# Kernel optimization log

Hardware: AMD Instinct MI355X
Metric: run time of the kernel (lower is better)

## Reference

```python
import jax, jax.numpy as jnp
import numpy as np

B, S, DM = 2, 2048, 2048
H, DH = 16, 128
EPS = 1e-6


def rmsnorm(t, w):
    # normalize over last dim (head_dim), fp32 math
    var = jnp.mean(jnp.square(t), axis=-1, keepdims=True)
    return t * jax.lax.rsqrt(var + EPS) * w


def apply_rope(t, freqs):
    # t: (B,S,H,D); freqs: (S,1,D/2,2,2)
    b, s, h, d = t.shape
    t2 = t.reshape(b, s, h, 2, d // 2)
    t2 = jnp.moveaxis(t2, -2, -1)[..., None, :]  # (B,S,H,D/2,1,2)
    out = freqs[..., 0] * t2[..., 0] + freqs[..., 1] * t2[..., 1]  # (B,S,H,D/2,2)
    out = jnp.moveaxis(out, -1, -2).reshape(b, s, h, d)
    return out.astype(t.dtype)


def setup_inputs() -> dict:
    key = jax.random.key(0)
    ks = jax.random.split(key, 6)
    sc = 0.02
    return {
        "x": jax.random.normal(ks[0], (B, S, DM), jnp.float32),
        "rope_emb": jax.random.normal(ks[1], (S, 1, DH // 2, 2, 2), jnp.float32),
        "wq": jax.random.normal(ks[2], (DM, DM), jnp.float32) * sc,
        "wk": jax.random.normal(ks[3], (DM, DM), jnp.float32) * sc,
        "wv": jax.random.normal(ks[4], (DM, DM), jnp.float32) * sc,
        "wo": jax.random.normal(ks[5], (DM, DM), jnp.float32) * sc,
        "q_norm_w": jnp.ones((DH,), jnp.float32),
        "k_norm_w": jnp.ones((DH,), jnp.float32),
    }


def reference(x, rope_emb, wq, wk, wv, wo, q_norm_w, k_norm_w):
    b, s, _ = x.shape
    q = (x @ wq.T).reshape(b, s, H, DH)
    k = (x @ wk.T).reshape(b, s, H, DH)
    v = (x @ wv.T).reshape(b, s, H, DH)
    q = rmsnorm(q, q_norm_w)
    k = rmsnorm(k, k_norm_w)
    q = apply_rope(q, rope_emb)
    k = apply_rope(k, rope_emb)
    scale = 1.0 / np.sqrt(DH).astype(np.float32)
    scores = jnp.einsum('bqhd,bkhd->bhqk', q, k) * scale
    attn = jax.nn.softmax(scores, axis=-1)
    out = jnp.einsum('bhqk,bkhd->bqhd', attn, v).reshape(b, s, H * DH)
    return out @ wo.T
```

## Files before the change

### kernel.cpp

```cpp
#include <hip/hip_runtime.h>

typedef __bf16 bf16x8 __attribute__((ext_vector_type(8)));
typedef __bf16 bf16x4 __attribute__((ext_vector_type(4)));
typedef float floatx4 __attribute__((ext_vector_type(4)));

#define GK 2048
#define S_LEN 2048
#define NH 16
#define DH 128

__device__ __forceinline__ void gl2lds16(const __bf16* g, __bf16* l) {
    __builtin_amdgcn_global_load_lds(
        (const __attribute__((address_space(1))) void*)g,
        (__attribute__((address_space(3))) void*)l, 16, 0, 0);
}

__global__ __launch_bounds__(256) void cvt_bf16(const float* __restrict__ in,
                                                __bf16* __restrict__ out, int n4) {
    int i = blockIdx.x * 256 + threadIdx.x;
    if (i < n4) {
        const float4 v = ((const float4*)in)[i];
        bf16x4 h;
        h[0] = (__bf16)v.x; h[1] = (__bf16)v.y; h[2] = (__bf16)v.z; h[3] = (__bf16)v.w;
        ((bf16x4*)out)[i] = h;
    }
}

__global__ __launch_bounds__(256) void cvt3_bf16(const float* __restrict__ a,
                                                 const float* __restrict__ b,
                                                 const float* __restrict__ c,
                                                 __bf16* __restrict__ out) {
    const int per = 2048 * 2048 / 4;
    int i = blockIdx.x * 256 + threadIdx.x;
    const float* src = a; int j = i;
    if (i >= 2 * per)      { src = c; j = i - 2 * per; }
    else if (i >= per)     { src = b; j = i - per; }
    const float4 v = ((const float4*)src)[j];
    bf16x4 h;
    h[0] = (__bf16)v.x; h[1] = (__bf16)v.y; h[2] = (__bf16)v.z; h[3] = (__bf16)v.w;
    ((bf16x4*)out)[i] = h;
}

__device__ __forceinline__ void gemm_body(const __bf16* __restrict__ A,
                                          const __bf16* __restrict__ W,
                                          int m0, int n0,
                                          __bf16 (*As)[32], __bf16 (*Bs)[32],
                                          floatx4 (*acc)[4]) {
    const int t = threadIdx.x, lane = t & 63, wave = t >> 6;
    const int fr = lane & 15, fq = lane >> 4;
    const int wr = (wave >> 1) * 64, wc = (wave & 1) * 64;

    const __bf16* Ap = A + (size_t)(m0 + wave * 32 + (lane >> 2)) * GK + (lane & 3) * 8;
    const __bf16* Wp = W + (size_t)(n0 + wave * 32 + (lane >> 2)) * GK + (lane & 3) * 8;
    __bf16* lA0 = &As[wave * 32][0];
    __bf16* lA1 = &As[wave * 32 + 16][0];
    __bf16* lB0 = &Bs[wave * 32][0];
    __bf16* lB1 = &Bs[wave * 32 + 16][0];

    for (int k0 = 0; k0 < GK; k0 += 32) {
        gl2lds16(Ap, lA0);
        gl2lds16(Ap + (size_t)16 * GK, lA1);
        gl2lds16(Wp, lB0);
        gl2lds16(Wp + (size_t)16 * GK, lB1);
        Ap += 32; Wp += 32;
        __syncthreads();

        bf16x8 af[4], bfg[4];
        for (int i = 0; i < 4; i++) af[i]  = *(const bf16x8*)&As[wr + i * 16 + fr][fq * 8];
        for (int j = 0; j < 4; j++) bfg[j] = *(const bf16x8*)&Bs[wc + j * 16 + fr][fq * 8];
        for (int i = 0; i < 4; i++)
            for (int j = 0; j < 4; j++)
                acc[i][j] = __builtin_amdgcn_mfma_f32_16x16x32_bf16(af[i], bfg[j], acc[i][j], 0, 0, 0);
        __syncthreads();
    }
}

__global__ __launch_bounds__(256) void gemm_qkv(const __bf16* __restrict__ A,
                                                const __bf16* __restrict__ W,
                                                __bf16* __restrict__ qb,
                                                __bf16* __restrict__ kb,
                                                __bf16* __restrict__ vbT) {
    __shared__ __align__(16) __bf16 As[128][32];
    __shared__ __align__(16) __bf16 Bs[128][32];
    const int m0 = blockIdx.y * 128, n0 = blockIdx.x * 128;
    floatx4 acc[4][4] = {};
    gemm_body(A, W, m0, n0, As, Bs, acc);

    const int lane = threadIdx.x & 63, wave = threadIdx.x >> 6;
    const int fr = lane & 15, fq = lane >> 4;
    const int wr = (wave >> 1) * 64, wc = (wave & 1) * 64;
    const int which = n0 >> 11;
    const int nc0 = n0 & 2047;

    for (int i = 0; i < 4; i++)
        for (int j = 0; j < 4; j++) {
            const int row = m0 + wr + i * 16 + fq * 4;
            const int col = nc0 + wc + j * 16 + fr;
            if (which == 2) {
                __bf16* Cp = vbT + (((size_t)(row & ~2047)) << 11) +
                             (size_t)col * 2048 + (row & 2047);
                bf16x4 hv;
                for (int r = 0; r < 4; r++) hv[r] = (__bf16)acc[i][j][r];
                *(bf16x4*)Cp = hv;
            } else {
                __bf16* dst = which ? kb : qb;
                for (int r = 0; r < 4; r++)
                    dst[(size_t)(row + r) * 2048 + col] = (__bf16)acc[i][j][r];
            }
        }
}

__global__ __launch_bounds__(256) void gemm_out(const __bf16* __restrict__ A,
                                                const __bf16* __restrict__ W,
                                                float* __restrict__ C) {
    __shared__ __align__(16) __bf16 As[128][32];
    __shared__ __align__(16) __bf16 Bs[128][32];
    const int m0 = blockIdx.y * 128, n0 = blockIdx.x * 128;
    floatx4 acc[4][4] = {};
    gemm_body(A, W, m0, n0, As, Bs, acc);

    const int lane = threadIdx.x & 63, wave = threadIdx.x >> 6;
    const int fr = lane & 15, fq = lane >> 4;
    const int wr = (wave >> 1) * 64, wc = (wave & 1) * 64;
    for (int i = 0; i < 4; i++)
        for (int j = 0; j < 4; j++) {
            const int row = m0 + wr + i * 16 + fq * 4;
            const int col = n0 + wc + j * 16 + fr;
            for (int r = 0; r < 4; r++)
                C[(size_t)(row + r) * 2048 + col] = acc[i][j][r];
        }
}

__global__ __launch_bounds__(256) void rmsrope(__bf16* __restrict__ qb,
                                               __bf16* __restrict__ kb,
                                               const float* __restrict__ rope,
                                               const float* __restrict__ qw,
                                               const float* __restrict__ kw) {
    const int lane = threadIdx.x & 63;
    const int row = blockIdx.x * 4 + (threadIdx.x >> 6);
    __bf16* p = (blockIdx.y ? kb : qb) + (size_t)row * DH;
    const float* w = blockIdx.y ? kw : qw;
    const int s = (row >> 4) & (S_LEN - 1);

    float t0 = (float)p[lane];
    float t1 = (float)p[lane + 64];
    float ss = t0 * t0 + t1 * t1;
    for (int o = 32; o; o >>= 1) ss += __shfl_xor(ss, o, 64);
    const float inv = rsqrtf(ss * (1.0f / 128.0f) + 1e-6f);
    t0 *= inv * w[lane];
    t1 *= inv * w[lane + 64];

    const float4 f = *(const float4*)(rope + (size_t)s * 256 + lane * 4);
    p[lane]      = (__bf16)(f.x * t0 + f.y * t1);
    p[lane + 64] = (__bf16)(f.z * t0 + f.w * t1);
}

__global__ __launch_bounds__(256) void flash(const __bf16* __restrict__ Q,
                                             const __bf16* __restrict__ K,
                                             const __bf16* __restrict__ Vt_g,
                                             __bf16* __restrict__ O) {
    __shared__ __align__(16) __bf16 Ks[32][136];
    __shared__ __align__(16) __bf16 Vt[144][40];
    __shared__ __align__(16) __bf16 Ps[4][32][40];

    const int t = threadIdx.x, lane = t & 63, wave = t >> 6;
    const int fr = lane & 15, fq = lane >> 4;
    const int b = blockIdx.y >> 4, h = blockIdx.y & 15;
    const size_t baseQ = (size_t)b * S_LEN * 2048 + h * 128;
    const size_t baseV = (size_t)b * 2048 * 2048 + (size_t)h * 128 * 2048;
    const int q0 = blockIdx.x * 128 + wave * 32;
    const float sc2 = 0.08838834764831845f * 1.4426950408889634f;
    const float M2 = 12.0f * 1.4426950408889634f;

    for (int idx = t; idx < 16 * 40; idx += 256) {
        const int rr = idx / 40, cc = idx - rr * 40;
        Vt[128 + rr][cc] = (rr == 0) ? (__bf16)1.0f : (__bf16)0.0f;
    }

    bf16x8 qf[2][4];
    for (int i2 = 0; i2 < 2; i2++) {
        const __bf16* qp = Q + baseQ + (size_t)(q0 + i2 * 16 + fr) * 2048 + fq * 8;
        for (int c = 0; c < 4; c++) qf[i2][c] = *(const bf16x8*)(qp + c * 32);
    }

    floatx4 oa[2][9] = {};

    const __bf16* Kp = K + baseQ + (size_t)(t >> 3) * 2048 + (t & 7) * 16;
    const __bf16* Vp = Vt_g + baseV + (size_t)(t >> 1) * 2048 + (t & 1) * 16;

    for (int kv0 = 0; kv0 < S_LEN; kv0 += 32) {
        *(uint4*)&Ks[t >> 3][(t & 7) * 16]     = *(const uint4*)(Kp);
        *(uint4*)&Ks[t >> 3][(t & 7) * 16 + 8] = *(const uint4*)(Kp + 8);
        *(uint4*)&Vt[t >> 1][(t & 1) * 16]     = *(const uint4*)(Vp);
        *(uint4*)&Vt[t >> 1][(t & 1) * 16 + 8] = *(const uint4*)(Vp + 8);
        Kp += (size_t)32 * 2048;
        Vp += 32;
        __syncthreads();

        floatx4 sacc[2][2] = {};
        for (int c = 0; c < 4; c++) {
            const bf16x8 kf0 = *(const bf16x8*)&Ks[fr][c * 32 + fq * 8];
            const bf16x8 kf1 = *(const bf16x8*)&Ks[fr + 16][c * 32 + fq * 8];
            sacc[0][0] = __builtin_amdgcn_mfma_f32_16x16x32_bf16(qf[0][c], kf0, sacc[0][0], 0, 0, 0);
            sacc[0][1] = __builtin_amdgcn_mfma_f32_16x16x32_bf16(qf[0][c], kf1, sacc[0][1], 0, 0, 0);
            sacc[1][0] = __builtin_amdgcn_mfma_f32_16x16x32_bf16(qf[1][c], kf0, sacc[1][0], 0, 0, 0);
            sacc[1][1] = __builtin_amdgcn_mfma_f32_16x16x32_bf16(qf[1][c], kf1, sacc[1][1], 0, 0, 0);
        }

        for (int i2 = 0; i2 < 2; i2++)
            for (int r = 0; r < 4; r++) {
                const int row = i2 * 16 + fq * 4 + r;
                Ps[wave][row][fr]      = (__bf16)exp2f(fmaf(sc2, sacc[i2][0][r], -M2));
                Ps[wave][row][fr + 16] = (__bf16)exp2f(fmaf(sc2, sacc[i2][1][r], -M2));
            }

        const bf16x8 pf0 = *(const bf16x8*)&Ps[wave][fr][fq * 8];
        const bf16x8 pf1 = *(const bf16x8*)&Ps[wave][16 + fr][fq * 8];
        for (int nb = 0; nb < 9; nb++) {
            const bf16x8 vf = *(const bf16x8*)&Vt[nb * 16 + fr][fq * 8];
            oa[0][nb] = __builtin_amdgcn_mfma_f32_16x16x32_bf16(pf0, vf, oa[0][nb], 0, 0, 0);
            oa[1][nb] = __builtin_amdgcn_mfma_f32_16x16x32_bf16(pf1, vf, oa[1][nb], 0, 0, 0);
        }
        __syncthreads();
    }

    for (int i2 = 0; i2 < 2; i2++)
        for (int r = 0; r < 4; r++) {
            float l = oa[i2][8][r];
            l = __shfl(l, fq * 16);
            const float inv = 1.0f / l;
            __bf16* op = O + baseQ + (size_t)(q0 + i2 * 16 + fq * 4 + r) * 2048;
            for (int nb = 0; nb < 8; nb++)
                op[nb * 16 + fr] = (__bf16)(oa[i2][nb][r] * inv);
        }
}

extern "C" void kernel_launch(void* const* d_in, const int* in_sizes, int n_in,
                              void* d_out, int out_size, void* d_ws, size_t ws_size,
                              hipStream_t stream) {
    const float* x    = (const float*)d_in[0];
    const float* rope = (const float*)d_in[1];
    const float* wq   = (const float*)d_in[2];
    const float* wk   = (const float*)d_in[3];
    const float* wv   = (const float*)d_in[4];
    const float* wo   = (const float*)d_in[5];
    const float* qnw  = (const float*)d_in[6];
    const float* knw  = (const float*)d_in[7];
    float* out = (float*)d_out;

    const size_t NTOK = 2 * 2048;
    const size_t ELEMS = NTOK * 2048;
    __bf16* xb  = (__bf16*)d_ws;
    __bf16* qb  = xb + ELEMS;
    __bf16* kb  = qb + ELEMS;
    __bf16* vbT = kb + ELEMS;
    __bf16* ob  = xb;
    __bf16* wqkv = (__bf16*)d_out;
    __bf16* wob  = qb;

    cvt_bf16<<<(int)(ELEMS / 4) / 256, 256, 0, stream>>>(x, xb, (int)(ELEMS / 4));
    cvt3_bf16<<<3 * (2048 * 2048 / 4) / 256, 256, 0, stream>>>(wq, wk, wv, wqkv);
    gemm_qkv<<<dim3(6144 / 128, (unsigned)(NTOK / 128)), 256, 0, stream>>>(xb, wqkv, qb, kb, vbT);
    rmsrope<<<dim3((unsigned)(NTOK * 16 / 4), 2), 256, 0, stream>>>(qb, kb, rope, qnw, knw);
    flash<<<dim3(S_LEN / 128, 2 * 16), 256, 0, stream>>>(qb, kb, vbT, ob);
    cvt_bf16<<<(int)(2048 * 2048 / 4) / 256, 256, 0, stream>>>(wo, wob, 2048 * 2048 / 4);
    gemm_out<<<dim3(2048 / 128, (unsigned)(NTOK / 128)), 256, 0, stream>>>(ob, wob, out);
}
```

Baseline: 452.5 us.

## Shrink flash tiles to 16 rows per wave, remap grid, vectorize rmsrope

The flash kernel now gives each wave 16 query rows instead of 32, so a block covers 64 queries and the grid grows to 1024 blocks. Block IDs are remapped so that neighbouring blocks share a batch-head, which should improve K/V cache reuse. V tiles are loaded with direct global-to-LDS transfers. rmsrope now uses 8-element vector loads and stores per thread, with shuffles to pair the rope halves. The finer tiling adds parallelism and lowers register pressure, but K/V are loaded twice as often per query row, and each loaded K/V tile feeds fewer MFMAs.

```diff
diff --git a/kernel.cpp b/kernel.cpp
--- a/kernel.cpp
+++ b/kernel.cpp
@@ -136,23 +136,37 @@
                                                const float* __restrict__ rope,
                                                const float* __restrict__ qw,
                                                const float* __restrict__ kw) {
-    const int lane = threadIdx.x & 63;
-    const int row = blockIdx.x * 4 + (threadIdx.x >> 6);
-    __bf16* p = (blockIdx.y ? kb : qb) + (size_t)row * DH;
-    const float* w = blockIdx.y ? kw : qw;
+    const int t = threadIdx.x;
+    const int row = blockIdx.x * 16 + (t >> 4);
+    const int c = t & 15;
+    __bf16* p = (blockIdx.y ? kb : qb) + (size_t)row * DH + c * 8;
+    const float* w = (blockIdx.y ? kw : qw) + c * 8;
     const int s = (row >> 4) & (S_LEN - 1);
 
-    float t0 = (float)p[lane];
-    float t1 = (float)p[lane + 64];
-    float ss = t0 * t0 + t1 * t1;
-    for (int o = 32; o; o >>= 1) ss += __shfl_xor(ss, o, 64);
+    const bf16x8 v = *(const bf16x8*)p;
+    float n[8];
+    float ss = 0.f;
+    for (int i = 0; i < 8; i++) { n[i] = (float)v[i]; ss += n[i] * n[i]; }
+    ss += __shfl_xor(ss, 1, 64);
+    ss += __shfl_xor(ss, 2, 64);
+    ss += __shfl_xor(ss, 4, 64);
+    ss += __shfl_xor(ss, 8, 64);
     const float inv = rsqrtf(ss * (1.0f / 128.0f) + 1e-6f);
-    t0 *= inv * w[lane];
-    t1 *= inv * w[lane + 64];
-
-    const float4 f = *(const float4*)(rope + (size_t)s * 256 + lane * 4);
-    p[lane]      = (__bf16)(f.x * t0 + f.y * t1);
-    p[lane + 64] = (__bf16)(f.z * t0 + f.w * t1);
+    const float4 w0 = *(const float4*)w, w1 = *(const float4*)(w + 4);
+    n[0] *= inv * w0.x; n[1] *= inv * w0.y; n[2] *= inv * w0.z; n[3] *= inv * w0.w;
+    n[4] *= inv * w1.x; n[5] *= inv * w1.y; n[6] *= inv * w1.z; n[7] *= inv * w1.w;
+
+    float pn[8];
+    for (int i = 0; i < 8; i++) pn[i] = __shfl_xor(n[i], 8, 64);
+
+    const float4* f = (const float4*)(rope + (size_t)s * 256 + (c & 7) * 32);
+    bf16x8 o;
+    if (c < 8) {
+        for (int i = 0; i < 8; i++) o[i] = (__bf16)(f[i].x * n[i] + f[i].y * pn[i]);
+    } else {
+        for (int i = 0; i < 8; i++) o[i] = (__bf16)(f[i].z * pn[i] + f[i].w * n[i]);
+    }
+    *(bf16x8*)p = o;
 }
 
 __global__ __launch_bounds__(256) void flash(const __bf16* __restrict__ Q,
@@ -160,79 +174,76 @@
                                              const __bf16* __restrict__ Vt_g,
                                              __bf16* __restrict__ O) {
     __shared__ __align__(16) __bf16 Ks[32][136];
-    __shared__ __align__(16) __bf16 Vt[144][40];
-    __shared__ __align__(16) __bf16 Ps[4][32][40];
+    __shared__ __align__(16) __bf16 Vt[144][32];
+    __shared__ __align__(16) __bf16 Ps[4][16][40];
 
     const int t = threadIdx.x, lane = t & 63, wave = t >> 6;
     const int fr = lane & 15, fq = lane >> 4;
-    const int b = blockIdx.y >> 4, h = blockIdx.y & 15;
+    const int id = blockIdx.x;
+    const int bh = (id & 7) + 8 * (id >> 8);
+    const int qidx = (id >> 3) & 31;
+    const int b = bh >> 4, h = bh & 15;
     const size_t baseQ = (size_t)b * S_LEN * 2048 + h * 128;
     const size_t baseV = (size_t)b * 2048 * 2048 + (size_t)h * 128 * 2048;
-    const int q0 = blockIdx.x * 128 + wave * 32;
+    const int q0 = qidx * 64 + wave * 16;
     const float sc2 = 0.08838834764831845f * 1.4426950408889634f;
     const float M2 = 12.0f * 1.4426950408889634f;
 
-    for (int idx = t; idx < 16 * 40; idx += 256) {
-        const int rr = idx / 40, cc = idx - rr * 40;
-        Vt[128 + rr][cc] = (rr == 0) ? (__bf16)1.0f : (__bf16)0.0f;
-    }
-
-    bf16x8 qf[2][4];
-    for (int i2 = 0; i2 < 2; i2++) {
-        const __bf16* qp = Q + baseQ + (size_t)(q0 + i2 * 16 + fr) * 2048 + fq * 8;
-        for (int c = 0; c < 4; c++) qf[i2][c] = *(const bf16x8*)(qp + c * 32);
-    }
-
-    floatx4 oa[2][9] = {};
+    for (int idx = t; idx < 16 * 32; idx += 256)
+        Vt[128 + (idx >> 5)][idx & 31] = ((idx >> 5) == 0) ? (__bf16)1.0f : (__bf16)0.0f;
+
+    bf16x8 qf[4];
+    {
+        const __bf16* qp = Q + baseQ + (size_t)(q0 + fr) * 2048 + fq * 8;
+        for (int c = 0; c < 4; c++) qf[c] = *(const bf16x8*)(qp + c * 32);
+    }
+
+    floatx4 oa[9] = {};
 
     const __bf16* Kp = K + baseQ + (size_t)(t >> 3) * 2048 + (t & 7) * 16;
-    const __bf16* Vp = Vt_g + baseV + (size_t)(t >> 1) * 2048 + (t & 1) * 16;
+    const __bf16* Vp = Vt_g + baseV + (size_t)(wave * 32 + (lane >> 2)) * 2048 + (lane & 3) * 8;
+    __bf16* lV0 = &Vt[wave * 32][0];
+    __bf16* lV1 = &Vt[wave * 32 + 16][0];
 
     for (int kv0 = 0; kv0 < S_LEN; kv0 += 32) {
         *(uint4*)&Ks[t >> 3][(t & 7) * 16]     = *(const uint4*)(Kp);
         *(uint4*)&Ks[t >> 3][(t & 7) * 16 + 8] = *(const uint4*)(Kp + 8);
-        *(uint4*)&Vt[t >> 1][(t & 1) * 16]     = *(const uint4*)(Vp);
-        *(uint4*)&Vt[t >> 1][(t & 1) * 16 + 8] = *(const uint4*)(Vp + 8);
+        gl2lds16(Vp, lV0);
+        gl2lds16(Vp + (size_t)16 * 2048, lV1);
         Kp += (size_t)32 * 2048;
         Vp += 32;
         __syncthreads();
 
-        floatx4 sacc[2][2] = {};
+        floatx4 s0 = {}, s1 = {};
         for (int c = 0; c < 4; c++) {
             const bf16x8 kf0 = *(const bf16x8*)&Ks[fr][c * 32 + fq * 8];
             const bf16x8 kf1 = *(const bf16x8*)&Ks[fr + 16][c * 32 + fq * 8];
-            sacc[0][0] = __builtin_amdgcn_mfma_f32_16x16x32_bf16(qf[0][c], kf0, sacc[0][0], 0, 0, 0);
-            sacc[0][1] = __builtin_amdgcn_mfma_f32_16x16x32_bf16(qf[0][c], kf1, sacc[0][1], 0, 0, 0);
-            sacc[1][0] = __builtin_amdgcn_mfma_f32_16x16x32_bf16(qf[1][c], kf0, sacc[1][0], 0, 0, 0);
-            sacc[1][1] = __builtin_amdgcn_mfma_f32_16x16x32_bf16(qf[1][c], kf1, sacc[1][1], 0, 0, 0);
-        }
-
-        for (int i2 = 0; i2 < 2; i2++)
-            for (int r = 0; r < 4; r++) {
-                const int row = i2 * 16 + fq * 4 + r;
-                Ps[wave][row][fr]      = (__bf16)exp2f(fmaf(sc2, sacc[i2][0][r], -M2));
-                Ps[wave][row][fr + 16] = (__bf16)exp2f(fmaf(sc2, sacc[i2][1][r], -M2));
-            }
-
-        const bf16x8 pf0 = *(const bf16x8*)&Ps[wave][fr][fq * 8];
-        const bf16x8 pf1 = *(const bf16x8*)&Ps[wave][16 + fr][fq * 8];
+            s0 = __builtin_amdgcn_mfma_f32_16x16x32_bf16(qf[c], kf0, s0, 0, 0, 0);
+            s1 = __builtin_amdgcn_mfma_f32_16x16x32_bf16(qf[c], kf1, s1, 0, 0, 0);
+        }
+
+        for (int r = 0; r < 4; r++) {
+            const int row = fq * 4 + r;
+            Ps[wave][row][fr]      = (__bf16)exp2f(fmaf(sc2, s0[r], -M2));
+            Ps[wave][row][fr + 16] = (__bf16)exp2f(fmaf(sc2, s1[r], -M2));
+        }
+
+        const bf16x8 pf = *(const bf16x8*)&Ps[wave][fr][fq * 8];
         for (int nb = 0; nb < 9; nb++) {
             const bf16x8 vf = *(const bf16x8*)&Vt[nb * 16 + fr][fq * 8];
-            oa[0][nb] = __builtin_amdgcn_mfma_f32_16x16x32_bf16(pf0, vf, oa[0][nb], 0, 0, 0);
-            oa[1][nb] = __builtin_amdgcn_mfma_f32_16x16x32_bf16(pf1, vf, oa[1][nb], 0, 0, 0);
-        }
-        __syncthreads();
-    }
-
-    for (int i2 = 0; i2 < 2; i2++)
-        for (int r = 0; r < 4; r++) {
-            float l = oa[i2][8][r];
-            l = __shfl(l, fq * 16);
-            const float inv = 1.0f / l;
-            __bf16* op = O + baseQ + (size_t)(q0 + i2 * 16 + fq * 4 + r) * 2048;
-            for (int nb = 0; nb < 8; nb++)
-                op[nb * 16 + fr] = (__bf16)(oa[i2][nb][r] * inv);
-        }
+            oa[nb] = __builtin_amdgcn_mfma_f32_16x16x32_bf16(pf, vf, oa[nb], 0, 0, 0);
+        }
+        __syncthreads();
+    }
+
+    for (int r = 0; r < 4; r++) {
+        float l = oa[8][r];
+        l = __shfl(l, fq * 16);
+        const float inv = 1.0f / l;
+        __bf16* op = O + baseQ + (size_t)(q0 + fq * 4 + r) * 2048;
+        for (int nb = 0; nb < 8; nb++)
+            op[nb * 16 + fr] = (__bf16)(oa[nb][r] * inv);
+    }
 }
 
 extern "C" void kernel_launch(void* const* d_in, const int* in_sizes, int n_in,
@@ -261,8 +272,8 @@
     cvt_bf16<<<(int)(ELEMS / 4) / 256, 256, 0, stream>>>(x, xb, (int)(ELEMS / 4));
     cvt3_bf16<<<3 * (2048 * 2048 / 4) / 256, 256, 0, stream>>>(wq, wk, wv, wqkv);
     gemm_qkv<<<dim3(6144 / 128, (unsigned)(NTOK / 128)), 256, 0, stream>>>(xb, wqkv, qb, kb, vbT);
-    rmsrope<<<dim3((unsigned)(NTOK * 16 / 4), 2), 256, 0, stream>>>(qb, kb, rope, qnw, knw);
-    flash<<<dim3(S_LEN / 128, 2 * 16), 256, 0, stream>>>(qb, kb, vbT, ob);
+    rmsrope<<<dim3((unsigned)(NTOK * NH / 16), 2), 256, 0, stream>>>(qb, kb, rope, qnw, knw);
+    flash<<<dim3(1024), 256, 0, stream>>>(qb, kb, vbT, ob);
     cvt_bf16<<<(int)(2048 * 2048 / 4) / 256, 256, 0, stream>>>(wo, wob, 2048 * 2048 / 4);
     gemm_out<<<dim3(2048 / 128, (unsigned)(NTOK / 128)), 256, 0, stream>>>(ob, wob, out);
 }
```

Result: slower. 487.8 us (+7.8%).
